# Optimization experiments

Measured on AMD Instinct MI355X. Metric: run time of the kernel, lower is better.

## Reference

```python
import jax, jax.numpy as jnp
import numpy as np

HIDDEN = 1024
HEADS = 16
HEAD_DIM = HIDDEN // HEADS
EPS = 1e-5


def setup_inputs() -> dict:
    key = jax.random.key(0)
    ks = jax.random.split(key, 9)
    B, S, H = 2, 2048, HIDDEN
    scale = 1.0 / np.sqrt(H)
    inp = {
        "hidden_states": jax.random.normal(ks[0], (B, S, H), dtype=jnp.float32),
        "Wq": jax.random.normal(ks[1], (H, H), dtype=jnp.float32) * scale,
        "bq": jnp.zeros((H,), jnp.float32),
        "Wk": jax.random.normal(ks[2], (H, H), dtype=jnp.float32) * scale,
        "bk": jnp.zeros((H,), jnp.float32),
        "Wv": jax.random.normal(ks[3], (H, H), dtype=jnp.float32) * scale,
        "bv": jnp.zeros((H,), jnp.float32),
        "Wo": jax.random.normal(ks[4], (H, H), dtype=jnp.float32) * scale,
        "bo": jnp.zeros((H,), jnp.float32),
        "gamma": jnp.ones((H,), jnp.float32),
        "beta": jnp.zeros((H,), jnp.float32),
    }
    return inp


def reference(hidden_states, Wq, bq, Wk, bk, Wv, bv, Wo, bo, gamma, beta):
    B, S, H = hidden_states.shape
    residual = hidden_states

    def shape(x):  # [B,S,H] -> [B,heads,S,head_dim]
        return x.reshape(B, S, HEADS, HEAD_DIM).transpose(0, 2, 1, 3)

    q = shape(hidden_states @ Wq + bq)
    k = shape(hidden_states @ Wk + bk)
    v = shape(hidden_states @ Wv + bv)

    scores = jnp.einsum("bhqd,bhkd->bhqk", q, k) / jnp.sqrt(
        jnp.asarray(HEAD_DIM, hidden_states.dtype))
    probs = jax.nn.softmax(scores, axis=-1)
    context = jnp.einsum("bhqk,bhkd->bhqd", probs, v)
    context = context.transpose(0, 2, 1, 3).reshape(B, S, H)

    output = context @ Wo + bo
    x = output + residual
    mu = jnp.mean(x, axis=-1, keepdims=True)
    var = jnp.mean(jnp.square(x - mu), axis=-1, keepdims=True)
    return (x - mu) * jax.lax.rsqrt(var + EPS) * gamma + beta
```

## Files before the change

kernel.cpp:

```cpp
#include <hip/hip_runtime.h>
#include <hip/hip_bf16.h>
#include <math.h>

#define HIDDEN 1024
#define HEADS 16
#define HEAD_DIM 64
#define EPS 1e-5f

typedef __attribute__((ext_vector_type(8))) short bf16x8;
typedef __attribute__((ext_vector_type(4))) float f32x4;

#if defined(__has_builtin)
#if __has_builtin(__builtin_amdgcn_exp2f)
#define EXP2(x) __builtin_amdgcn_exp2f(x)
#endif
#endif
#ifndef EXP2
#define EXP2(x) exp2f(x)
#endif

#define QSCALE 0.18033688011112042f

__device__ __forceinline__ short f2bf(float f) {
    union { float f; unsigned u; } v; v.f = f;
    unsigned r = v.u + 0x7fffu + ((v.u >> 16) & 1u);
    return (short)(r >> 16);
}

__device__ __forceinline__ void gl_lds16(const void* g, void* l) {
    __builtin_amdgcn_global_load_lds(
        (const __attribute__((address_space(1))) void*)g,
        (__attribute__((address_space(3))) void*)l, 16, 0, 0);
}

__global__ __launch_bounds__(256) void cast_bf16_kernel(
    const float* __restrict__ in, short* __restrict__ out, int n)
{
    int i = (blockIdx.x * 256 + threadIdx.x) * 4;
    if (i >= n) return;
    float4 v = *(const float4*)(in + i);
    short o[4] = { f2bf(v.x), f2bf(v.y), f2bf(v.z), f2bf(v.w) };
    *(uint2*)(out + i) = *(uint2*)o;
}

__global__ __launch_bounds__(256) void wtrans_kernel(
    const float* __restrict__ Wq, const float* __restrict__ Wk,
    const float* __restrict__ Wv, const float* __restrict__ Wo,
    short* __restrict__ Wt3, short* __restrict__ Wot)
{
    const int wsel = blockIdx.z;
    const float* W = (wsel == 0) ? Wq : (wsel == 1) ? Wk : (wsel == 2) ? Wv : Wo;
    short* dst = (wsel < 3) ? (Wt3 + (size_t)wsel * 1024 * 1024) : Wot;
    const float scale = (wsel == 0) ? QSCALE : 1.0f;

    __shared__ short tile[32][33];
    int n0 = blockIdx.x * 32;
    int k0 = blockIdx.y * 32;
    int tx = threadIdx.x & 31;
    int ty = threadIdx.x >> 5;
    #pragma unroll
    for (int i = 0; i < 32; i += 8)
        tile[ty + i][tx] = f2bf(W[(size_t)(k0 + ty + i) * 1024 + n0 + tx] * scale);
    __syncthreads();
    #pragma unroll
    for (int i = 0; i < 32; i += 8)
        dst[(size_t)(n0 + ty + i) * 1024 + k0 + tx] = tile[tx][ty + i];
}

__global__ __launch_bounds__(256) void concat_bias_kernel(
    const float* __restrict__ bq, const float* __restrict__ bk,
    const float* __restrict__ bv, float* __restrict__ b3)
{
    int i = blockIdx.x * 256 + threadIdx.x;
    if (i >= 3072) return;
    float v = (i < 1024) ? bq[i] * QSCALE
            : (i < 2048) ? bk[i - 1024] : bv[i - 2048];
    b3[i] = v;
}

template<int BM>
__global__ __launch_bounds__(256) void gemm_bt_mfma(
    const short* __restrict__ A, const short* __restrict__ Bt,
    const float* __restrict__ bias,
    void* __restrict__ C0, int ldc0,
    void* __restrict__ C1, int split_col, int ldc1,
    const float* __restrict__ resid,
    int M, int N, int K, int out_bf16)
{
    constexpr int MT = BM / 32;
    constexpr int ACH = BM / 32;
    __shared__ short As[BM * 64];
    __shared__ short Bs[128 * 64];
    const int tid = threadIdx.x;
    const int wave = tid >> 6, lane = tid & 63;
    const int ln16 = lane & 15, quad = lane >> 4;
    const int wm = (wave >> 1) * (BM / 2), wn = (wave & 1) * 64;

    const int gx = gridDim.x;
    int bid = blockIdx.y * gx + blockIdx.x;
    const int cpx = (gx * gridDim.y) >> 3;
    bid = (bid & 7) * cpx + (bid >> 3);
    const int brow = (bid / gx) * BM, bcol = (bid % gx) * 128;

    const int kr  = lane >> 3;
    const int kb8 = lane & 7;

    f32x4 acc[MT][4];
    #pragma unroll
    for (int mt = 0; mt < MT; ++mt)
        #pragma unroll
        for (int nt = 0; nt < 4; ++nt) acc[mt][nt] = (f32x4){0.f, 0.f, 0.f, 0.f};

    for (int k0 = 0; k0 < K; k0 += 64) {
        __syncthreads();
        #pragma unroll
        for (int i = 0; i < ACH; ++i) {
            int ci = wave * ACH + i;
            int r  = ci * 8 + kr;
            int csrc = (kb8 ^ (r & 7)) * 8;
            gl_lds16(A + (size_t)(brow + r) * K + k0 + csrc, As + ci * 512);
        }
        #pragma unroll
        for (int i = 0; i < 4; ++i) {
            int ci = wave * 4 + i;
            int r  = ci * 8 + kr;
            int csrc = (kb8 ^ (r & 7)) * 8;
            gl_lds16(Bt + (size_t)(bcol + r) * K + k0 + csrc, Bs + ci * 512);
        }
        __syncthreads();

        #pragma unroll
        for (int kk = 0; kk < 2; ++kk) {
            bf16x8 af[MT], bf[4];
            #pragma unroll
            for (int mt = 0; mt < MT; ++mt) {
                int r = wm + mt * 16 + ln16;
                af[mt] = *(const bf16x8*)&As[r * 64 + (((kk * 4 + quad) ^ (r & 7)) * 8)];
            }
            #pragma unroll
            for (int nt = 0; nt < 4; ++nt) {
                int r = wn + nt * 16 + ln16;
                bf[nt] = *(const bf16x8*)&Bs[r * 64 + (((kk * 4 + quad) ^ (r & 7)) * 8)];
            }
            #pragma unroll
            for (int mt = 0; mt < MT; ++mt)
                #pragma unroll
                for (int nt = 0; nt < 4; ++nt)
                    acc[mt][nt] = __builtin_amdgcn_mfma_f32_16x16x32_bf16(
                        af[mt], bf[nt], acc[mt][nt], 0, 0, 0);
        }
    }

    void* Cp = C0; int ld = ldc0; int coff = 0;
    if (bcol >= split_col) { Cp = C1; ld = ldc1; coff = split_col; }

    #pragma unroll
    for (int mt = 0; mt < MT; ++mt) {
        #pragma unroll
        for (int r = 0; r < 4; ++r) {
            int row = brow + wm + mt * 16 + quad * 4 + r;
            #pragma unroll
            for (int nt = 0; nt < 4; ++nt) {
                int col = bcol + wn + nt * 16 + ln16;
                float v = acc[mt][nt][r] + bias[col];
                if (resid) v += resid[(size_t)row * N + col];
                if (out_bf16) ((short*)Cp)[(size_t)row * ld + (col - coff)] = f2bf(v);
                else          ((float*)Cp)[(size_t)row * ld + (col - coff)] = v;
            }
        }
    }
}

__global__ __launch_bounds__(256) void vtranspose_kernel(
    const short* __restrict__ Vb, short* __restrict__ VT)
{
    __shared__ short t[64][72];
    const int c0 = blockIdx.x * 64;
    const int r0 = blockIdx.y * 64;
    const int tid = threadIdx.x;
    #pragma unroll
    for (int i = 0; i < 2; ++i) {
        int idx = tid + i * 256;
        int r = idx >> 3, cc = (idx & 7) * 8;
        *(uint4*)&t[r][cc] = *(const uint4*)(Vb + (size_t)(r0 + r) * 1024 + c0 + cc);
    }
    __syncthreads();
    #pragma unroll
    for (int i = 0; i < 2; ++i) {
        int idx = tid + i * 256;
        int c = idx >> 3, rr = (idx & 7) * 8;
        short tmp[8];
        #pragma unroll
        for (int j = 0; j < 8; ++j) tmp[j] = t[rr + j][c];
        *(uint4*)(VT + (size_t)(c0 + c) * 4096 + r0 + rr) = *(uint4*)tmp;
    }
}

__global__ __launch_bounds__(256, 3) void attn_mfma_kernel(
    const short* __restrict__ QKb, const short* __restrict__ VT,
    short* __restrict__ Ctx)
{
    const int S = 2048;
    const int h = blockIdx.x, qt = blockIdx.y, b = blockIdx.z;
    const int tid = threadIdx.x;
    const int wave = tid >> 6, lane = tid & 63;
    const int ln16 = lane & 15, quad = lane >> 4;

    __shared__ alignas(16) char smem[32768];
    short* Ks = (short*)smem;
    short* Vs = (short*)(smem + 16384);
    char*  Pw = smem + wave * 4096;

    bf16x8 qf[4][2];
    #pragma unroll
    for (int qg = 0; qg < 4; ++qg)
        #pragma unroll
        for (int kb = 0; kb < 2; ++kb)
            qf[qg][kb] = *(const bf16x8*)(QKb +
                (size_t)(b * S + qt * 64 + qg * 16 + ln16) * 2048 +
                h * 64 + kb * 32 + quad * 8);

    f32x4 of[4][4];
    float rs[4] = {0.f, 0.f, 0.f, 0.f};
    #pragma unroll
    for (int qg = 0; qg < 4; ++qg)
        #pragma unroll
        for (int nt = 0; nt < 4; ++nt) of[qg][nt] = (f32x4){0.f, 0.f, 0.f, 0.f};

    auto stage = [&](int kt) {
        const int kr  = lane >> 3;
        const int kb8 = lane & 7;
        const int vr  = lane >> 4;
        const int vb16 = lane & 15;
        #pragma unroll
        for (int i = 0; i < 4; ++i) {
            int r = wave * 32 + i * 8 + kr;
            int ksrc = (kb8 ^ (r & 7)) * 8;
            gl_lds16(QKb + (size_t)(b * S + kt * 128 + r) * 2048 + 1024 + h * 64 + ksrc,
                     Ks + (wave * 32 + i * 8) * 64);
            int d = wave * 16 + i * 4 + vr;
            int vsrc = (vb16 ^ (d & 15)) * 8;
            gl_lds16(VT + (size_t)(h * 64 + d) * 4096 + b * S + kt * 128 + vsrc,
                     Vs + (wave * 16 + i * 4) * 128);
        }
    };

    for (int kt = 0; kt < 16; ++kt) {
        if (kt) __syncthreads();
        stage(kt);
        __syncthreads();

        const int t0w = wave * 32;

        bf16x8 kf[2][2];
        #pragma unroll
        for (int kblk = 0; kblk < 2; ++kblk) {
            int rloc = t0w + kblk * 16 + ln16;
            kf[kblk][0] = *(const bf16x8*)&Ks[rloc * 64 + ((quad ^ (rloc & 7)) * 8)];
            kf[kblk][1] = *(const bf16x8*)&Ks[rloc * 64 + (((4 + quad) ^ (rloc & 7)) * 8)];
        }

        #pragma unroll
        for (int kblk = 0; kblk < 2; ++kblk) {
            #pragma unroll
            for (int qg = 0; qg < 4; ++qg) {
                f32x4 a = (f32x4){0.f, 0.f, 0.f, 0.f};
                __builtin_amdgcn_s_setprio(1);
                a = __builtin_amdgcn_mfma_f32_16x16x32_bf16(kf[kblk][0], qf[qg][0], a, 0, 0, 0);
                a = __builtin_amdgcn_mfma_f32_16x16x32_bf16(kf[kblk][1], qf[qg][1], a, 0, 0, 0);
                __builtin_amdgcn_s_setprio(0);
                float p0 = EXP2(a[0]), p1 = EXP2(a[1]);
                float p2 = EXP2(a[2]), p3 = EXP2(a[3]);
                rs[qg] += (p0 + p1) + (p2 + p3);
                union { __hip_bfloat162 h2; unsigned u; } c01, c23;
                c01.h2 = __float22bfloat162_rn(make_float2(p0, p1));
                c23.h2 = __float22bfloat162_rn(make_float2(p2, p3));
                uint2 w; w.x = c01.u; w.y = c23.u;
                int qrow = qg * 16 + ln16;
                int key = (qrow >> 1) & 3;
                int bblk = (kblk * 2 + (quad >> 1)) ^ key;
                *(uint2*)(Pw + qrow * 64 + bblk * 16 + (quad & 1) * 8) = w;
            }
        }

        bf16x8 pf[4];
        #pragma unroll
        for (int qg = 0; qg < 4; ++qg) {
            int qrow = qg * 16 + ln16;
            int key = (qrow >> 1) & 3;
            pf[qg] = *(const bf16x8*)(Pw + qrow * 64 + ((quad ^ key) * 16));
        }
        __builtin_amdgcn_s_setprio(1);
        #pragma unroll
        for (int nt = 0; nt < 4; ++nt) {
            int d = nt * 16 + ln16;
            bf16x8 vf = *(const bf16x8*)&Vs[d * 128 + (((wave * 4 + quad) ^ (d & 15)) * 8)];
            #pragma unroll
            for (int qg = 0; qg < 4; ++qg)
                of[qg][nt] = __builtin_amdgcn_mfma_f32_16x16x32_bf16(pf[qg], vf, of[qg][nt], 0, 0, 0);
        }
        __builtin_amdgcn_s_setprio(0);
    }

    __syncthreads();

    #pragma unroll
    for (int qg = 0; qg < 4; ++qg) {
        rs[qg] += __shfl_xor(rs[qg], 16, 64);
        rs[qg] += __shfl_xor(rs[qg], 32, 64);
    }

    float* Rw = (float*)(smem + wave * 4864);
    float* Lb = (float*)(smem + 4 * 4864);

    if (quad == 0) {
        #pragma unroll
        for (int qg = 0; qg < 4; ++qg)
            Lb[wave * 64 + qg * 16 + ln16] = rs[qg];
    }

    const int rq  = tid >> 2;
    const int rd0 = (tid & 3) * 4;
    float inv = 0.f;

    #pragma unroll
    for (int nt = 0; nt < 4; ++nt) {
        #pragma unroll
        for (int qg = 0; qg < 4; ++qg)
            #pragma unroll
            for (int r = 0; r < 4; ++r)
                Rw[(qg * 16 + quad * 4 + r) * 19 + ln16] = of[qg][nt][r];
        __syncthreads();
        if (nt == 0) {
            float l = Lb[rq] + Lb[64 + rq] + Lb[128 + rq] + Lb[192 + rq];
            inv = 1.f / l;
        }
        short o4[4];
        #pragma unroll
        for (int j = 0; j < 4; ++j) {
            int d = rd0 + j;
            float s = 0.f;
            #pragma unroll
            for (int w = 0; w < 4; ++w)
                s += ((const float*)(smem + w * 4864))[rq * 19 + d];
            o4[j] = f2bf(s * inv);
        }
        *(uint2*)(Ctx + (size_t)(b * S + qt * 64 + rq) * 1024 + h * 64 + nt * 16 + rd0) =
            *(uint2*)o4;
        __syncthreads();
    }
}

__global__ __launch_bounds__(256) void resln_kernel(
    const float* __restrict__ xin, const float* __restrict__ gamma,
    const float* __restrict__ beta, float* __restrict__ out)
{
    const int row = blockIdx.x;
    const int tid = threadIdx.x;
    const int wid = tid >> 6, lane = tid & 63;
    __shared__ float red[8];

    float4 x = *(const float4*)(xin + (size_t)row * HIDDEN + tid * 4);
    float s = x.x + x.y + x.z + x.w;
    #pragma unroll
    for (int off = 32; off > 0; off >>= 1) s += __shfl_xor(s, off, 64);
    if (lane == 0) red[wid] = s;
    __syncthreads();
    float mu = (red[0] + red[1] + red[2] + red[3]) * (1.f / HIDDEN);

    float dx = x.x - mu, dy = x.y - mu, dz = x.z - mu, dw = x.w - mu;
    float v = dx * dx + dy * dy + dz * dz + dw * dw;
    #pragma unroll
    for (int off = 32; off > 0; off >>= 1) v += __shfl_xor(v, off, 64);
    if (lane == 0) red[4 + wid] = v;
    __syncthreads();
    float var = (red[4] + red[5] + red[6] + red[7]) * (1.f / HIDDEN);
    float rstd = rsqrtf(var + EPS);

    float4 g = *(const float4*)(gamma + tid * 4);
    float4 bt = *(const float4*)(beta + tid * 4);
    float4 o;
    o.x = dx * rstd * g.x + bt.x;
    o.y = dy * rstd * g.y + bt.y;
    o.z = dz * rstd * g.z + bt.z;
    o.w = dw * rstd * g.w + bt.w;
    *(float4*)(out + (size_t)row * HIDDEN + tid * 4) = o;
}

extern "C" void kernel_launch(void* const* d_in, const int* in_sizes, int n_in,
                              void* d_out, int out_size, void* d_ws, size_t ws_size,
                              hipStream_t stream)
{
    const float* X     = (const float*)d_in[0];
    const float* Wq    = (const float*)d_in[1];
    const float* bq    = (const float*)d_in[2];
    const float* Wk    = (const float*)d_in[3];
    const float* bk    = (const float*)d_in[4];
    const float* Wv    = (const float*)d_in[5];
    const float* bv    = (const float*)d_in[6];
    const float* Wo    = (const float*)d_in[7];
    const float* bo    = (const float*)d_in[8];
    const float* gamma = (const float*)d_in[9];
    const float* beta  = (const float*)d_in[10];
    float* out = (float*)d_out;

    const int B = 2, S = 2048;
    const int M = B * S;
    const size_t mat = (size_t)M * HIDDEN;

    char* ws = (char*)d_ws;
    short* Xb  = (short*)(ws);
    short* VT  = (short*)(ws);
    short* Wot = (short*)(ws + (8ull << 20));
    short* Wt3 = (short*)(ws + (10ull << 20));
    float* b3  = (float*)(ws + (16ull << 20));
    short* QKb = (short*)(ws + (17ull << 20));
    float* Pj  = (float*)(ws + (17ull << 20));
    short* Vb  = (short*)(ws + (33ull << 20));
    short* Ctx = (short*)(ws + (33ull << 20));

    dim3 blk(256);

    cast_bf16_kernel<<<dim3((int)(mat / 4 / 256)), blk, 0, stream>>>(X, Xb, (int)mat);
    wtrans_kernel<<<dim3(32, 32, 4), blk, 0, stream>>>(Wq, Wk, Wv, Wo, Wt3, Wot);
    concat_bias_kernel<<<12, blk, 0, stream>>>(bq, bk, bv, b3);

    dim3 qkvgrid(3072 / 128, M / 128);
    gemm_bt_mfma<128><<<qkvgrid, blk, 0, stream>>>(Xb, Wt3, b3,
                                              QKb, 2048, Vb, 2048, 1024,
                                              nullptr, M, 3072, HIDDEN, 1);

    vtranspose_kernel<<<dim3(16, 64), blk, 0, stream>>>(Vb, VT);

    dim3 agrid(HEADS, S / 64, B);
    attn_mfma_kernel<<<agrid, blk, 0, stream>>>(QKb, VT, Ctx);

    dim3 ogrid(HIDDEN / 128, M / 64);
    gemm_bt_mfma<64><<<ogrid, blk, 0, stream>>>(Ctx, Wot, bo,
                                            Pj, 1024, nullptr, 1 << 30, 0,
                                            X, M, HIDDEN, HIDDEN, 0);

    resln_kernel<<<M, blk, 0, stream>>>(Pj, gamma, beta, out);
}
```

Before: 231.4 us.

## Fuse prep kernels and double-buffer GEMM and attention LDS staging

Merges the X cast, weight transpose and bias concat into one prep launch, removing two kernel launches. The GEMM now double-buffers its A/B LDS tiles so the next tile's global-to-LDS loads are issued while the current tile is multiplied, leaving one barrier per iteration. The attention kernel moves the P scratch into its own LDS region, loads the V fragments before the barrier and then prefetches the next K/V tile while computing. It also reorders the QK MFMAs so they are batched across query groups. These changes double LDS use, which may lower occupancy. The async LDS loads also rely on the barrier ordering being correct.

```diff
diff --git a/kernel.cpp b/kernel.cpp
--- a/kernel.cpp
+++ b/kernel.cpp
@@ -33,49 +33,44 @@
         (__attribute__((address_space(3))) void*)l, 16, 0, 0);
 }
 
-__global__ __launch_bounds__(256) void cast_bf16_kernel(
-    const float* __restrict__ in, short* __restrict__ out, int n)
-{
-    int i = (blockIdx.x * 256 + threadIdx.x) * 4;
-    if (i >= n) return;
-    float4 v = *(const float4*)(in + i);
-    short o[4] = { f2bf(v.x), f2bf(v.y), f2bf(v.z), f2bf(v.w) };
-    *(uint2*)(out + i) = *(uint2*)o;
-}
-
-__global__ __launch_bounds__(256) void wtrans_kernel(
+__global__ __launch_bounds__(256) void prep_kernel(
+    const float* __restrict__ X,
     const float* __restrict__ Wq, const float* __restrict__ Wk,
     const float* __restrict__ Wv, const float* __restrict__ Wo,
-    short* __restrict__ Wt3, short* __restrict__ Wot)
-{
-    const int wsel = blockIdx.z;
-    const float* W = (wsel == 0) ? Wq : (wsel == 1) ? Wk : (wsel == 2) ? Wv : Wo;
-    short* dst = (wsel < 3) ? (Wt3 + (size_t)wsel * 1024 * 1024) : Wot;
-    const float scale = (wsel == 0) ? QSCALE : 1.0f;
-
+    const float* __restrict__ bq, const float* __restrict__ bk,
+    const float* __restrict__ bv,
+    short* __restrict__ Xb, short* __restrict__ Wt3, short* __restrict__ Wot,
+    float* __restrict__ b3)
+{
+    const int z = blockIdx.z;
     __shared__ short tile[32][33];
-    int n0 = blockIdx.x * 32;
-    int k0 = blockIdx.y * 32;
-    int tx = threadIdx.x & 31;
-    int ty = threadIdx.x >> 5;
-    #pragma unroll
-    for (int i = 0; i < 32; i += 8)
-        tile[ty + i][tx] = f2bf(W[(size_t)(k0 + ty + i) * 1024 + n0 + tx] * scale);
-    __syncthreads();
-    #pragma unroll
-    for (int i = 0; i < 32; i += 8)
-        dst[(size_t)(n0 + ty + i) * 1024 + k0 + tx] = tile[tx][ty + i];
-}
-
-__global__ __launch_bounds__(256) void concat_bias_kernel(
-    const float* __restrict__ bq, const float* __restrict__ bk,
-    const float* __restrict__ bv, float* __restrict__ b3)
-{
-    int i = blockIdx.x * 256 + threadIdx.x;
-    if (i >= 3072) return;
-    float v = (i < 1024) ? bq[i] * QSCALE
-            : (i < 2048) ? bk[i - 1024] : bv[i - 2048];
-    b3[i] = v;
+    if (z < 4) {
+        const float* W = (z == 0) ? Wq : (z == 1) ? Wk : (z == 2) ? Wv : Wo;
+        short* dst = (z < 3) ? (Wt3 + (size_t)z * 1024 * 1024) : Wot;
+        const float scale = (z == 0) ? QSCALE : 1.0f;
+        int n0 = blockIdx.x * 32, k0 = blockIdx.y * 32;
+        int tx = threadIdx.x & 31, ty = threadIdx.x >> 5;
+        #pragma unroll
+        for (int i = 0; i < 32; i += 8)
+            tile[ty + i][tx] = f2bf(W[(size_t)(k0 + ty + i) * 1024 + n0 + tx] * scale);
+        __syncthreads();
+        #pragma unroll
+        for (int i = 0; i < 32; i += 8)
+            dst[(size_t)(n0 + ty + i) * 1024 + k0 + tx] = tile[tx][ty + i];
+    } else if (z < 8) {
+        int l = (z - 4) * 1024 + blockIdx.y * 32 + blockIdx.x;
+        int i = (l * 256 + threadIdx.x) * 4;
+        float4 v = *(const float4*)(X + i);
+        short o[4] = { f2bf(v.x), f2bf(v.y), f2bf(v.z), f2bf(v.w) };
+        *(uint2*)(Xb + i) = *(uint2*)o;
+    } else {
+        int i = (blockIdx.y * 32 + blockIdx.x) * 256 + threadIdx.x;
+        if (i < 3072) {
+            float v = (i < 1024) ? bq[i] * QSCALE
+                    : (i < 2048) ? bk[i - 1024] : bv[i - 2048];
+            b3[i] = v;
+        }
+    }
 }
 
 template<int BM>
@@ -89,8 +84,8 @@
 {
     constexpr int MT = BM / 32;
     constexpr int ACH = BM / 32;
-    __shared__ short As[BM * 64];
-    __shared__ short Bs[128 * 64];
+    __shared__ short As[2][BM * 64];
+    __shared__ short Bs[2][128 * 64];
     const int tid = threadIdx.x;
     const int wave = tid >> 6, lane = tid & 63;
     const int ln16 = lane & 15, quad = lane >> 4;
@@ -111,23 +106,30 @@
         #pragma unroll
         for (int nt = 0; nt < 4; ++nt) acc[mt][nt] = (f32x4){0.f, 0.f, 0.f, 0.f};
 
-    for (int k0 = 0; k0 < K; k0 += 64) {
-        __syncthreads();
+    auto stage = [&](int p, int kt) {
         #pragma unroll
         for (int i = 0; i < ACH; ++i) {
             int ci = wave * ACH + i;
             int r  = ci * 8 + kr;
             int csrc = (kb8 ^ (r & 7)) * 8;
-            gl_lds16(A + (size_t)(brow + r) * K + k0 + csrc, As + ci * 512);
+            gl_lds16(A + (size_t)(brow + r) * K + kt * 64 + csrc, &As[p][ci * 512]);
         }
         #pragma unroll
         for (int i = 0; i < 4; ++i) {
             int ci = wave * 4 + i;
             int r  = ci * 8 + kr;
             int csrc = (kb8 ^ (r & 7)) * 8;
-            gl_lds16(Bt + (size_t)(bcol + r) * K + k0 + csrc, Bs + ci * 512);
-        }
-        __syncthreads();
+            gl_lds16(Bt + (size_t)(bcol + r) * K + kt * 64 + csrc, &Bs[p][ci * 512]);
+        }
+    };
+
+    const int NKT = K / 64;
+    stage(0, 0);
+    __syncthreads();
+
+    for (int kt = 0; kt < NKT; ++kt) {
+        const int cur = kt & 1;
+        if (kt + 1 < NKT) stage(cur ^ 1, kt + 1);
 
         #pragma unroll
         for (int kk = 0; kk < 2; ++kk) {
@@ -135,12 +137,12 @@
             #pragma unroll
             for (int mt = 0; mt < MT; ++mt) {
                 int r = wm + mt * 16 + ln16;
-                af[mt] = *(const bf16x8*)&As[r * 64 + (((kk * 4 + quad) ^ (r & 7)) * 8)];
+                af[mt] = *(const bf16x8*)&As[cur][r * 64 + (((kk * 4 + quad) ^ (r & 7)) * 8)];
             }
             #pragma unroll
             for (int nt = 0; nt < 4; ++nt) {
                 int r = wn + nt * 16 + ln16;
-                bf[nt] = *(const bf16x8*)&Bs[r * 64 + (((kk * 4 + quad) ^ (r & 7)) * 8)];
+                bf[nt] = *(const bf16x8*)&Bs[cur][r * 64 + (((kk * 4 + quad) ^ (r & 7)) * 8)];
             }
             #pragma unroll
             for (int mt = 0; mt < MT; ++mt)
@@ -149,6 +151,7 @@
                     acc[mt][nt] = __builtin_amdgcn_mfma_f32_16x16x32_bf16(
                         af[mt], bf[nt], acc[mt][nt], 0, 0, 0);
         }
+        __syncthreads();
     }
 
     void* Cp = C0; int ld = ldc0; int coff = 0;
@@ -206,10 +209,10 @@
     const int wave = tid >> 6, lane = tid & 63;
     const int ln16 = lane & 15, quad = lane >> 4;
 
-    __shared__ alignas(16) char smem[32768];
+    __shared__ alignas(16) char smem[49152];
     short* Ks = (short*)smem;
     short* Vs = (short*)(smem + 16384);
-    char*  Pw = smem + wave * 4096;
+    char*  Pw = smem + 32768 + wave * 4096;
 
     bf16x8 qf[4][2];
     #pragma unroll
@@ -245,32 +248,44 @@
         }
     };
 
+    stage(0);
+    __syncthreads();
+
+    const int t0w = wave * 32;
+
     for (int kt = 0; kt < 16; ++kt) {
-        if (kt) __syncthreads();
-        stage(kt);
-        __syncthreads();
-
-        const int t0w = wave * 32;
-
-        bf16x8 kf[2][2];
+        bf16x8 kf[2][2], vf[4];
         #pragma unroll
         for (int kblk = 0; kblk < 2; ++kblk) {
             int rloc = t0w + kblk * 16 + ln16;
             kf[kblk][0] = *(const bf16x8*)&Ks[rloc * 64 + ((quad ^ (rloc & 7)) * 8)];
             kf[kblk][1] = *(const bf16x8*)&Ks[rloc * 64 + (((4 + quad) ^ (rloc & 7)) * 8)];
         }
+        #pragma unroll
+        for (int nt = 0; nt < 4; ++nt) {
+            int d = nt * 16 + ln16;
+            vf[nt] = *(const bf16x8*)&Vs[d * 128 + (((wave * 4 + quad) ^ (d & 15)) * 8)];
+        }
+        __syncthreads();
+        if (kt + 1 < 16) stage(kt + 1);
 
         #pragma unroll
         for (int kblk = 0; kblk < 2; ++kblk) {
+            f32x4 a[4];
+            __builtin_amdgcn_s_setprio(1);
             #pragma unroll
             for (int qg = 0; qg < 4; ++qg) {
-                f32x4 a = (f32x4){0.f, 0.f, 0.f, 0.f};
-                __builtin_amdgcn_s_setprio(1);
-                a = __builtin_amdgcn_mfma_f32_16x16x32_bf16(kf[kblk][0], qf[qg][0], a, 0, 0, 0);
-                a = __builtin_amdgcn_mfma_f32_16x16x32_bf16(kf[kblk][1], qf[qg][1], a, 0, 0, 0);
-                __builtin_amdgcn_s_setprio(0);
-                float p0 = EXP2(a[0]), p1 = EXP2(a[1]);
-                float p2 = EXP2(a[2]), p3 = EXP2(a[3]);
+                a[qg] = (f32x4){0.f, 0.f, 0.f, 0.f};
+                a[qg] = __builtin_amdgcn_mfma_f32_16x16x32_bf16(kf[kblk][0], qf[qg][0], a[qg], 0, 0, 0);
+            }
+            #pragma unroll
+            for (int qg = 0; qg < 4; ++qg)
+                a[qg] = __builtin_amdgcn_mfma_f32_16x16x32_bf16(kf[kblk][1], qf[qg][1], a[qg], 0, 0, 0);
+            __builtin_amdgcn_s_setprio(0);
+            #pragma unroll
+            for (int qg = 0; qg < 4; ++qg) {
+                float p0 = EXP2(a[qg][0]), p1 = EXP2(a[qg][1]);
+                float p2 = EXP2(a[qg][2]), p3 = EXP2(a[qg][3]);
                 rs[qg] += (p0 + p1) + (p2 + p3);
                 union { __hip_bfloat162 h2; unsigned u; } c01, c23;
                 c01.h2 = __float22bfloat162_rn(make_float2(p0, p1));
@@ -292,17 +307,14 @@
         }
         __builtin_amdgcn_s_setprio(1);
         #pragma unroll
-        for (int nt = 0; nt < 4; ++nt) {
-            int d = nt * 16 + ln16;
-            bf16x8 vf = *(const bf16x8*)&Vs[d * 128 + (((wave * 4 + quad) ^ (d & 15)) * 8)];
+        for (int nt = 0; nt < 4; ++nt)
             #pragma unroll
             for (int qg = 0; qg < 4; ++qg)
-                of[qg][nt] = __builtin_amdgcn_mfma_f32_16x16x32_bf16(pf[qg], vf, of[qg][nt], 0, 0, 0);
-        }
+                of[qg][nt] = __builtin_amdgcn_mfma_f32_16x16x32_bf16(pf[qg], vf[nt], of[qg][nt], 0, 0, 0);
         __builtin_amdgcn_s_setprio(0);
-    }
-
-    __syncthreads();
+
+        __syncthreads();
+    }
 
     #pragma unroll
     for (int qg = 0; qg < 4; ++qg) {
@@ -407,6 +419,7 @@
     const int B = 2, S = 2048;
     const int M = B * S;
     const size_t mat = (size_t)M * HIDDEN;
+    (void)mat;
 
     char* ws = (char*)d_ws;
     short* Xb  = (short*)(ws);
@@ -421,9 +434,8 @@
 
     dim3 blk(256);
 
-    cast_bf16_kernel<<<dim3((int)(mat / 4 / 256)), blk, 0, stream>>>(X, Xb, (int)mat);
-    wtrans_kernel<<<dim3(32, 32, 4), blk, 0, stream>>>(Wq, Wk, Wv, Wo, Wt3, Wot);
-    concat_bias_kernel<<<12, blk, 0, stream>>>(bq, bk, bv, b3);
+    prep_kernel<<<dim3(32, 32, 9), blk, 0, stream>>>(
+        X, Wq, Wk, Wv, Wo, bq, bk, bv, Xb, Wt3, Wot, b3);
 
     dim3 qkvgrid(3072 / 128, M / 128);
     gemm_bt_mfma<128><<<qkvgrid, blk, 0, stream>>>(Xb, Wt3, b3,
```

Measured after the change: 260.6 us. 1.13x slower.
